# Kernel optimization log

Hardware: AMD Instinct MI355X
Metric: run time of the kernel (lower is better)

## Reference

```python
import jax, jax.numpy as jnp
import numpy as np

D_MODEL = 512
D_STATE = 128
D_CONV = 4
EXPAND = 2
HEADDIM = 64
D_INNER = EXPAND * D_MODEL            # 1024
NHEADS = D_INNER // HEADDIM           # 16
CONV_DIM = D_INNER + 2 * D_STATE      # 1280
D_IN_PROJ = 2 * D_INNER + 2 * D_STATE + NHEADS  # 2320
EPS = 1e-5


def _mamba2(u, in_w, conv_w, conv_b, A_log, dt_bias, Dp, norm_w, out_w):
    # u: [b, l, d_model]  -- Mamba2 forward (ngroups=1), SSD in exact quadratic form
    b, l, _ = u.shape
    zxbcdt = u @ in_w.T                                   # [b,l,2320]
    z = zxbcdt[..., :D_INNER]
    xBC = zxbcdt[..., D_INNER:D_INNER + CONV_DIM]
    dt = zxbcdt[..., D_INNER + CONV_DIM:]                 # [b,l,nheads]
    # causal depthwise conv1d (kernel 4) + silu
    xp = jnp.pad(xBC, ((0, 0), (D_CONV - 1, 0), (0, 0)))
    conv = sum(xp[:, k:k + l, :] * conv_w[:, k] for k in range(D_CONV))
    xBC = jax.nn.silu(conv + conv_b)
    x = xBC[..., :D_INNER].reshape(b, l, NHEADS, HEADDIM)
    Bm = xBC[..., D_INNER:D_INNER + D_STATE]              # [b,l,d_state]
    Cm = xBC[..., D_INNER + D_STATE:]                     # [b,l,d_state]
    dt = jax.nn.softplus(dt + dt_bias)                    # [b,l,nheads]
    dtA = dt * (-jnp.exp(A_log))                          # [b,l,nheads], negative
    # SSD quadratic (semiseparable) form: L[t,s] = exp(sum_{r=s+1..t} dtA_r), causal
    cs = jnp.cumsum(dtA, axis=1)                          # [b,l,nh]
    seg = cs[:, :, None, :] - cs[:, None, :, :]           # [b,t,s,nh]
    mask = jnp.tril(jnp.ones((l, l), bool))
    L = jnp.exp(jnp.where(mask[None, :, :, None], seg, -jnp.inf))
    G = jnp.einsum('btd,bsd->bts', Cm, Bm)                # C_t . B_s
    dtx = dt[..., None] * x                               # [b,l,nh,hd]
    y = jnp.einsum('btsn,bsnp->btnp', G[..., None] * L, dtx)
    y = (y + x * Dp[:, None]).reshape(b, l, D_INNER)      # D skip
    # gated RMSNorm (norm_before_gate=False): rmsnorm(y * silu(z)) * weight
    y = y * jax.nn.silu(z)
    y = y * jax.lax.rsqrt(jnp.mean(jnp.square(y), -1, keepdims=True) + EPS) * norm_w
    return y @ out_w.T


def _forward(x, h_in_w, h_conv_w, h_conv_b, h_A_log, h_dt_bias, h_D, h_norm_w, h_out_w,
             v_in_w, v_conv_w, v_conv_b, v_A_log, v_dt_bias, v_D, v_norm_w, v_out_w,
             fc_w, fc_b):
    B, H, W, C = x.shape
    hp = (h_in_w, h_conv_w, h_conv_b, h_A_log, h_dt_bias, h_D, h_norm_w, h_out_w)
    vp = (v_in_w, v_conv_w, v_conv_b, v_A_log, v_dt_bias, v_D, v_norm_w, v_out_w)
    # horizontal: scan along W for each (B*H) row
    xh = x.reshape(-1, W, C)
    h1 = _mamba2(xh, *hp)
    # NOTE: original code flips dim 0 (batch), reproduced faithfully
    h2 = jnp.flip(_mamba2(jnp.flip(xh, 0), *hp), 0)
    h = jnp.concatenate([h1, h2], -1).reshape(B, H, W, -1)
    # vertical: scan along H for each (B*W) column
    xv = jnp.transpose(x, (0, 2, 1, 3)).reshape(-1, H, C)
    v1 = _mamba2(xv, *vp)
    v2 = jnp.flip(_mamba2(jnp.flip(xv, 0), *vp), 0)
    v = jnp.transpose(jnp.concatenate([v1, v2], -1).reshape(B, W, H, -1), (0, 2, 1, 3))
    out = jnp.concatenate([v, h], -1) @ fc_w.T + fc_b     # [B,H,W,C]
    return out


def setup_inputs() -> dict:
    key = jax.random.key(0)
    ks = jax.random.split(key, 8)
    B, H, W, C = 2, 64, 64, D_MODEL
    x = jax.random.normal(ks[0], (B, H, W, C), jnp.float32)

    def mk(k):
        kk = jax.random.split(k, 5)
        return {
            'in_w': 0.02 * jax.random.normal(kk[0], (D_IN_PROJ, D_MODEL), jnp.float32),
            'conv_w': 0.1 * jax.random.normal(kk[1], (CONV_DIM, D_CONV), jnp.float32),
            'conv_b': jnp.zeros((CONV_DIM,), jnp.float32),
            'A_log': jnp.log(jax.random.uniform(kk[2], (NHEADS,), jnp.float32, 1.0, 16.0)),
            'dt_bias': jnp.log(jnp.expm1(jax.random.uniform(kk[3], (NHEADS,), jnp.float32, 1e-3, 0.1))),
            'D': jnp.ones((NHEADS,), jnp.float32),
            'norm_w': jnp.ones((D_INNER,), jnp.float32),
            'out_w': 0.02 * jax.random.normal(kk[4], (D_MODEL, D_INNER), jnp.float32),
        }

    hp, vp = mk(ks[1]), mk(ks[2])
    inp = {'x': x}
    inp.update({f'h_{n}': v for n, v in hp.items()})
    inp.update({f'v_{n}': v for n, v in vp.items()})
    inp['fc_w'] = 0.02 * jax.random.normal(ks[3], (D_MODEL, 4 * D_MODEL), jnp.float32)
    inp['fc_b'] = jnp.zeros((D_MODEL,), jnp.float32)
    return inp


def reference(x, h_in_w, h_conv_w, h_conv_b, h_A_log, h_dt_bias, h_D, h_norm_w, h_out_w,
              v_in_w, v_conv_w, v_conv_b, v_A_log, v_dt_bias, v_D, v_norm_w, v_out_w,
              fc_w, fc_b):
    return _forward(x, h_in_w, h_conv_w, h_conv_b, h_A_log, h_dt_bias, h_D, h_norm_w, h_out_w,
                    v_in_w, v_conv_w, v_conv_b, v_A_log, v_dt_bias, v_D, v_norm_w, v_out_w,
                    fc_w, fc_b)
```

## Files before the change

### kernel.cpp

```cpp
#include <hip/hip_runtime.h>

#define NROWS 8192
#define NZX   2304
#define BCS   136
#define XMS   72

#define PB0 4096
#define PB1 (PB0 + 2048)
#define PB2 (PB1 + 2304)
#define PB3 (PB2 + 256)
#define PB4 (PB3 + 512)

typedef __attribute__((ext_vector_type(8))) short bf16x8;
typedef __attribute__((ext_vector_type(4))) float f32x4;

__device__ __forceinline__ float bf2f(unsigned short u) {
    union { unsigned int i; float f; } v; v.i = ((unsigned int)u) << 16; return v.f;
}
__device__ __forceinline__ unsigned short f2bf(float f) {
    union { float f; unsigned int i; } v; v.f = f;
    return (unsigned short)((v.i + 0x8000u) >> 16);
}

__device__ __forceinline__ void async_lds16(const unsigned short* g, unsigned short* l) {
    __builtin_amdgcn_global_load_lds(
        (const __attribute__((address_space(1))) unsigned int*)g,
        (__attribute__((address_space(3))) unsigned int*)l, 16, 0, 0);
}

__global__ __launch_bounds__(256) void prep_kernel(
    const float* __restrict__ x, const float* __restrict__ fcw,
    const float* __restrict__ iw0, const float* __restrict__ iw1,
    const float* __restrict__ ow0, const float* __restrict__ ow1,
    const float* __restrict__ db0, const float* __restrict__ db1,
    const float* __restrict__ al0, const float* __restrict__ al1,
    unsigned short* __restrict__ xbf, unsigned short* __restrict__ wf,
    unsigned short* __restrict__ wbA, unsigned short* __restrict__ wbOT0,
    unsigned short* __restrict__ wbOT1, float* __restrict__ dtbb,
    float* __restrict__ csbb)
{
    __shared__ char sm[37888] __attribute__((aligned(16)));
    const int blk = blockIdx.x, tid = threadIdx.x;
    if (blk < PB0) {
        int i = blk * 256 + tid;
        float4 v = *(const float4*)(x + (size_t)i * 4);
        ushort4 o;
        o.x = f2bf(v.x); o.y = f2bf(v.y); o.z = f2bf(v.z); o.w = f2bf(v.w);
        *(ushort4*)(xbf + (size_t)i * 4) = o;
    } else if (blk < PB1) {
        int idx = (blk - PB0) * 256 + tid;
        int o = idx >> 10, c = idx & 1023;
        int half = c >> 9, cc = c & 511;
        float v = fcw[(size_t)o * 2048 + half * 1024 + cc] +
                  fcw[(size_t)o * 2048 + half * 1024 + 512 + cc];
        wf[idx] = f2bf(v);
    } else if (blk < PB2) {
        int local = blk - PB1;
        int dir = local / 1152;
        int i = (local % 1152) * 256 + tid;
        const float* s = dir ? iw1 : iw0;
        float4 v = *(const float4*)(s + (size_t)i * 4);
        ushort4 o;
        o.x = f2bf(v.x); o.y = f2bf(v.y); o.z = f2bf(v.z); o.w = f2bf(v.w);
        *(ushort4*)(wbA + (size_t)dir * (2304 * 512) + (size_t)i * 4) = o;
    } else if (blk < PB3) {
        float (*T)[65] = (float(*)[65])sm;
        int local = blk - PB2;
        int z = local >> 7, rem = local & 127;
        const float* s = z ? ow1 : ow0;
        unsigned short* d = z ? wbOT1 : wbOT0;
        const int bo = (rem >> 4) * 64, bc = (rem & 15) * 64;
#pragma unroll
        for (int i = 0; i < 16; ++i) {
            int slot = tid + i * 256;
            int r = slot >> 6, c = slot & 63;
            T[r][c] = s[(size_t)(bo + r) * 1024 + bc + c];
        }
        __syncthreads();
#pragma unroll
        for (int i = 0; i < 16; ++i) {
            int slot = tid + i * 256;
            int cr = slot >> 6, oc = slot & 63;
            d[(size_t)(bc + cr) * 512 + bo + oc] = f2bf(T[oc][cr]);
        }
    } else {
        float (*wsm)[512] = (float(*)[512])sm;
        float (*xs)[68]   = (float(*)[68])(sm + 16384);
        float (*dta)[64]  = (float(*)[64])(sm + 16384 + 17408);
        float (*dtt)[64]  = (float(*)[64])(sm + 16384 + 17408 + 2048);
        int local = blk - PB3;
        const int dir = local >> 8, bxl = local & 255;
        const float* in_w = dir ? iw1 : iw0;
        const float* dt_bias = dir ? db1 : db0;
        const float* A_log = dir ? al1 : al0;
        float* dtb = dtbb + (size_t)dir * 131072;
        float* csb = csbb + (size_t)dir * 131072;
        const int seq = bxl >> 1, hq = bxl & 1;
#pragma unroll
        for (int i = 0; i < 4; ++i) {
            int slot = tid + i * 256;
            int h = slot >> 7, c = (slot & 127) * 4;
            *(float4*)&wsm[h][c] = *(const float4*)(in_w + (size_t)(2304 + hq * 8 + h) * 512 + c);
        }
        const int t = tid & 63, hg = tid >> 6;
        float acc[2] = {0.f, 0.f};
        for (int c0 = 0; c0 < 512; c0 += 64) {
            __syncthreads();
#pragma unroll
            for (int i = 0; i < 4; ++i) {
                int slot = tid + i * 256;
                int r = slot >> 4, cc = (slot & 15) * 4;
                size_t row = (dir == 0) ? (size_t)seq * 64 + r
                                        : (size_t)(seq >> 6) * 4096 + (size_t)r * 64 + (seq & 63);
                *(float4*)&xs[r][cc] = *(const float4*)(x + row * 512 + c0 + cc);
            }
            __syncthreads();
#pragma unroll
            for (int cc = 0; cc < 64; cc += 4) {
                float4 u4 = *(const float4*)&xs[t][cc];
                const float* w0 = &wsm[hg * 2][c0 + cc];
                const float* w1 = &wsm[hg * 2 + 1][c0 + cc];
                acc[0] += u4.x * w0[0] + u4.y * w0[1] + u4.z * w0[2] + u4.w * w0[3];
                acc[1] += u4.x * w1[0] + u4.y * w1[1] + u4.z * w1[2] + u4.w * w1[3];
            }
        }
#pragma unroll
        for (int hh = 0; hh < 2; ++hh) {
            int hl = hg * 2 + hh;
            int h = hq * 8 + hl;
            float v = acc[hh] + dt_bias[h];
            float dtv = (v > 20.f) ? v : log1pf(__expf(v));
            dtt[hl][t] = dtv;
            dta[hl][t] = dtv * -__expf(A_log[h]);
        }
        __syncthreads();
        if (tid < 8) {
            float run = 0.f;
            int ob = (seq * 16 + hq * 8 + tid) * 64;
            for (int tt = 0; tt < 64; ++tt) {
                run += dta[tid][tt];
                dtb[ob + tt] = dtt[tid][tt];
                csb[ob + tt] = run;
            }
        }
    }
}

__global__ __launch_bounds__(256) void gemm_phase(
    const unsigned short* __restrict__ xbf, const unsigned short* __restrict__ wbA,
    unsigned short* __restrict__ zx, const unsigned short* __restrict__ wf,
    const unsigned short* __restrict__ wbOT0, const unsigned short* __restrict__ wbOT1,
    unsigned short* __restrict__ wcomb)
{
    __shared__ unsigned short SMEM[16384];
    unsigned short* As = SMEM;
    unsigned short* Bs = SMEM + 8192;
    const int bx = blockIdx.x, by = blockIdx.y, z = blockIdx.z;
    const unsigned short *A, *B;
    unsigned short* C;
    int lda, ldb, ldc, perm, mB, nB;
    if (bx < 64) {
        A = xbf; lda = 512; perm = z;
        B = wbA + (size_t)z * (2304 * 512); ldb = 512;
        C = zx + (size_t)z * NROWS * NZX; ldc = NZX;
        mB = bx * 128; nB = by * 128;
    } else {
        if (by >= 8) return;
        A = z ? wf : wf + 512; lda = 1024; perm = 0;
        B = z ? wbOT1 : wbOT0; ldb = 512;
        C = z ? wcomb : wcomb + 1024; ldc = 2048;
        mB = (bx - 64) * 128; nB = by * 128;
    }
    const int tid = threadIdx.x, wave = tid >> 6, lane = tid & 63;
    const int wm = (wave >> 1) * 64, wn = (wave & 1) * 64;
    const int lr = lane & 15, lq = lane >> 4;
    const unsigned short* AgP[4];
    const unsigned short* BgP[4];
    unsigned short* lA[4];
    unsigned short* lB[4];
#pragma unroll
    for (int i = 0; i < 4; ++i) {
        int s = tid + i * 256;
        int r = s >> 3, p = s & 7;
        int q = p ^ (r & 7);
        int ar = mB + r;
        if (perm) ar = (ar & ~4095) | ((ar & 63) << 6) | ((ar >> 6) & 63);
        AgP[i] = A + (size_t)ar * lda + q * 8;
        BgP[i] = B + (size_t)(nB + r) * ldb + q * 8;
        lA[i] = As + s * 8;
        lB[i] = Bs + s * 8;
    }
    const int aswz = lr & 7;
    int arb[4], brb[4];
#pragma unroll
    for (int i = 0; i < 4; ++i) {
        arb[i] = (wm + i * 16 + lr) * 64;
        brb[i] = (wn + i * 16 + lr) * 64;
    }
    f32x4 zero4 = {0.f,0.f,0.f,0.f};
    f32x4 acc[4][4] = {{zero4,zero4,zero4,zero4},{zero4,zero4,zero4,zero4},
                       {zero4,zero4,zero4,zero4},{zero4,zero4,zero4,zero4}};
    for (int k0 = 0; k0 < 512; k0 += 64) {
#pragma unroll
        for (int i = 0; i < 4; ++i) async_lds16(AgP[i] + k0, lA[i]);
#pragma unroll
        for (int i = 0; i < 4; ++i) async_lds16(BgP[i] + k0, lB[i]);
        __syncthreads();
#pragma unroll
        for (int kh = 0; kh < 2; ++kh) {
            const int ksw = ((kh * 4 + lq) ^ aswz) * 8;
            bf16x8 a[4], b[4];
#pragma unroll
            for (int i = 0; i < 4; ++i) a[i] = *(const bf16x8*)(As + arb[i] + ksw);
#pragma unroll
            for (int i = 0; i < 4; ++i) b[i] = *(const bf16x8*)(Bs + brb[i] + ksw);
#pragma unroll
            for (int mi = 0; mi < 4; ++mi)
#pragma unroll
                for (int ni = 0; ni < 4; ++ni)
                    acc[mi][ni] = __builtin_amdgcn_mfma_f32_16x16x32_bf16(
                        a[mi], b[ni], acc[mi][ni], 0, 0, 0);
        }
        __syncthreads();
    }
    unsigned short* WR = SMEM + wave * 1024;
#pragma unroll
    for (int mi = 0; mi < 4; ++mi) {
#pragma unroll
        for (int ni = 0; ni < 4; ++ni) {
#pragma unroll
            for (int r = 0; r < 4; ++r) {
                int r16 = lq * 4 + r;
                int cn = ni * 16 + lr;
                int gp = ((cn >> 3) + (r16 >> 1)) & 7;
                WR[r16 * 64 + gp * 8 + (cn & 7)] = f2bf(acc[mi][ni][r]);
            }
        }
#pragma unroll
        for (int j = 0; j < 2; ++j) {
            int r16 = j * 8 + (lane >> 3);
            int gr = lane & 7;
            int gp = (gr + (r16 >> 1)) & 7;
            uint4 v = *(const uint4*)(WR + r16 * 64 + gp * 8);
            int row = mB + wm + mi * 16 + r16;
            *(uint4*)(C + (size_t)row * ldc + nB + wn + gr * 8) = v;
        }
    }
}

__global__ __launch_bounds__(256) void gemm_final2048(
    const unsigned short* __restrict__ YV, const unsigned short* __restrict__ YH,
    const unsigned short* __restrict__ W, const float* __restrict__ bias,
    float* __restrict__ C)
{
    __shared__ unsigned short As[128 * 64];
    __shared__ unsigned short Bs[64 * 64];
    const int tid = threadIdx.x, wave = tid >> 6, lane = tid & 63;
    const int mB = blockIdx.x * 128, nB = blockIdx.y * 64;
    const int lr = lane & 15, lq = lane >> 4;
    int aq[4], agr[4], apr[4];
    unsigned short* lA[4];
    const unsigned short* BgP[2];
    unsigned short* lB[2];
#pragma unroll
    for (int i = 0; i < 4; ++i) {
        int s = tid + i * 256;
        int r = s >> 3, p = s & 7;
        aq[i] = (p ^ (r & 7)) * 8;
        int gr = mB + r;
        agr[i] = gr;
        apr[i] = (gr & ~4095) | ((gr & 63) << 6) | ((gr >> 6) & 63);
        lA[i] = As + s * 8;
    }
#pragma unroll
    for (int i = 0; i < 2; ++i) {
        int s = tid + i * 256;
        int r = s >> 3, p = s & 7;
        int q = p ^ (r & 7);
        BgP[i] = W + (size_t)(nB + r) * 2048 + q * 8;
        lB[i] = Bs + s * 8;
    }
    const int aswz = lr & 7;
    int arb[2], brb[4];
#pragma unroll
    for (int i = 0; i < 2; ++i) arb[i] = (wave * 32 + i * 16 + lr) * 64;
#pragma unroll
    for (int i = 0; i < 4; ++i) brb[i] = (i * 16 + lr) * 64;
    f32x4 zero4 = {0.f,0.f,0.f,0.f};
    f32x4 acc[2][4] = {{zero4,zero4,zero4,zero4},{zero4,zero4,zero4,zero4}};
    for (int k0 = 0; k0 < 2048; k0 += 64) {
#pragma unroll
        for (int i = 0; i < 4; ++i) {
            int kk = k0 + aq[i];
            const unsigned short* g = (kk < 1024)
                ? YV + (size_t)apr[i] * 1024 + kk
                : YH + (size_t)agr[i] * 1024 + (kk - 1024);
            async_lds16(g, lA[i]);
        }
#pragma unroll
        for (int i = 0; i < 2; ++i) async_lds16(BgP[i] + k0, lB[i]);
        __syncthreads();
#pragma unroll
        for (int kh = 0; kh < 2; ++kh) {
            const int ksw = ((kh * 4 + lq) ^ aswz) * 8;
            bf16x8 a[2], b[4];
#pragma unroll
            for (int i = 0; i < 2; ++i) a[i] = *(const bf16x8*)(As + arb[i] + ksw);
#pragma unroll
            for (int i = 0; i < 4; ++i) b[i] = *(const bf16x8*)(Bs + brb[i] + ksw);
#pragma unroll
            for (int mi = 0; mi < 2; ++mi)
#pragma unroll
                for (int ni = 0; ni < 4; ++ni)
                    acc[mi][ni] = __builtin_amdgcn_mfma_f32_16x16x32_bf16(
                        a[mi], b[ni], acc[mi][ni], 0, 0, 0);
        }
        __syncthreads();
    }
    const int rbase = lq * 4;
#pragma unroll
    for (int mi = 0; mi < 2; ++mi)
#pragma unroll
        for (int ni = 0; ni < 4; ++ni) {
            int col = nB + ni * 16 + lr;
            float bb = bias[col];
#pragma unroll
            for (int r = 0; r < 4; ++r) {
                int row = mB + wave * 32 + mi * 16 + rbase + r;
                C[(size_t)row * 512 + col] = acc[mi][ni][r] + bb;
            }
        }
}

__global__ __launch_bounds__(320) void conv_silu(
    const unsigned short* __restrict__ zxb, const float* __restrict__ cw0,
    const float* __restrict__ cw1, const float* __restrict__ cb0,
    const float* __restrict__ cb1, unsigned short* __restrict__ xbcb)
{
    __shared__ unsigned short S[64 * 320];
    const int dir = blockIdx.y;
    const unsigned short* zx = zxb + (size_t)dir * NROWS * NZX;
    unsigned short* xbc = xbcb + (size_t)dir * NROWS * 1280;
    const float* cw = dir ? cw1 : cw0;
    const float* cb = dir ? cb1 : cb0;
    const int tid = threadIdx.x;
    const int seq = blockIdx.x >> 2, tile = blockIdx.x & 3;
    const int cbase = tile * 320;
    const unsigned short* src = zx + (size_t)seq * 64 * NZX + 1024 + cbase;
#pragma unroll
    for (int i = 0; i < 8; ++i) {
        int slot = tid + i * 320;
        int r = slot / 40, ch = (slot % 40) * 8;
        *(uint4*)(S + r * 320 + ch) = *(const uint4*)(src + (size_t)r * NZX + ch);
    }
    __syncthreads();
    const int c8 = (tid % 40) * 8, rg = tid / 40;
    const int gc = cbase + c8;
    float4 b0 = *(const float4*)(cb + gc), b1 = *(const float4*)(cb + gc + 4);
    const float bias[8] = {b0.x,b0.y,b0.z,b0.w,b1.x,b1.y,b1.z,b1.w};
    float4 wv[8];
#pragma unroll
    for (int j = 0; j < 8; ++j) wv[j] = *(const float4*)(cw + (size_t)(gc + j) * 4);
    unsigned short* dst = xbc + (size_t)seq * 64 * 1280 + gc;
#pragma unroll
    for (int r = 0; r < 8; ++r) {
        int t = rg * 8 + r;
        float acc[8];
#pragma unroll
        for (int j = 0; j < 8; ++j) acc[j] = bias[j];
#pragma unroll
        for (int k = 0; k < 4; ++k) {
            int ts = t + k - 3;
            if (ts >= 0) {
                uint4 xv = *(const uint4*)(S + ts * 320 + c8);
                const unsigned short* xs = (const unsigned short*)&xv;
#pragma unroll
                for (int j = 0; j < 8; ++j)
                    acc[j] += bf2f(xs[j]) * ((const float*)&wv[j])[k];
            }
        }
        unsigned short out8[8] __attribute__((aligned(16)));
#pragma unroll
        for (int j = 0; j < 8; ++j) out8[j] = f2bf(acc[j] / (1.f + __expf(-acc[j])));
        *(uint4*)(dst + (size_t)t * 1280) = *(const uint4*)out8;
    }
}

__global__ __launch_bounds__(256) void gmat_kernel(
    const unsigned short* __restrict__ xbcb, float* __restrict__ Gbuf)
{
    __shared__ unsigned short Bs[64 * BCS];
    __shared__ unsigned short Cs[64 * BCS];
    const int dir = blockIdx.y, seq = blockIdx.x;
    const unsigned short* base = xbcb + (size_t)dir * NROWS * 1280
                                      + (size_t)seq * 64 * 1280;
    const int tid = threadIdx.x;
    const int lane = tid & 63, wave = tid >> 6;
#pragma unroll
    for (int i = 0; i < 4; ++i) {
        int e = (tid + i * 256) * 8;
        int r = e >> 7, c = e & 127;
        *(uint4*)(Bs + r * BCS + c) = *(const uint4*)(base + (size_t)r * 1280 + 1024 + c);
        *(uint4*)(Cs + r * BCS + c) = *(const uint4*)(base + (size_t)r * 1280 + 1152 + c);
    }
    __syncthreads();
    const int lr = lane & 15, lq = lane >> 4;
    f32x4 zero4 = {0.f,0.f,0.f,0.f};
    f32x4 acc[4] = {zero4, zero4, zero4, zero4};
#pragma unroll
    for (int kt = 0; kt < 4; ++kt) {
        bf16x8 a = *(const bf16x8*)(Cs + (wave * 16 + lr) * BCS + kt * 32 + lq * 8);
#pragma unroll
        for (int ni = 0; ni < 4; ++ni) {
            bf16x8 b = *(const bf16x8*)(Bs + (ni * 16 + lr) * BCS + kt * 32 + lq * 8);
            acc[ni] = __builtin_amdgcn_mfma_f32_16x16x32_bf16(a, b, acc[ni], 0, 0, 0);
        }
    }
    float* G = Gbuf + ((size_t)dir * 128 + seq) * 4096;
#pragma unroll
    for (int ni = 0; ni < 4; ++ni) {
        int s = ni * 16 + lr;
#pragma unroll
        for (int r = 0; r < 4; ++r) {
            int t = wave * 16 + lq * 4 + r;
            G[t * 64 + s] = acc[ni][r];
        }
    }
}

__global__ __launch_bounds__(256) void scan_kernel(
    const unsigned short* __restrict__ xbcb, const float* __restrict__ Gbuf,
    const float* __restrict__ dtbb, const float* __restrict__ csbb,
    const float* __restrict__ Dv0, const float* __restrict__ Dv1,
    unsigned short* __restrict__ yh, unsigned short* __restrict__ yv)
{
    __shared__ unsigned short XsT[64 * XMS];
    __shared__ unsigned short Ms[64 * XMS];
    __shared__ float dts[64], css[64];
    const int dir = blockIdx.y;
    const unsigned short* xbc = xbcb + (size_t)dir * NROWS * 1280;
    const float* dtb = dtbb + (size_t)dir * 131072;
    const float* csb = csbb + (size_t)dir * 131072;
    const float* Dv = dir ? Dv1 : Dv0;
    unsigned short* y = dir ? yv : yh;
    const int tid = threadIdx.x;
    const int lane = tid & 63, wave = tid >> 6;
    const int seq = blockIdx.x >> 4, h = blockIdx.x & 15;
    if (tid < 64) {
        dts[tid] = dtb[(seq * 16 + h) * 64 + tid];
        css[tid] = csb[(seq * 16 + h) * 64 + tid];
    }
    const unsigned short* base = xbc + (size_t)seq * 64 * 1280;
#pragma unroll
    for (int i = 0; i < 2; ++i) {
        int e = (tid + i * 256) * 8;
        int t = e >> 6, p0 = e & 63;
        uint4 xval = *(const uint4*)(base + (size_t)t * 1280 + h * 64 + p0);
        const unsigned short* xs = (const unsigned short*)&xval;
#pragma unroll
        for (int j = 0; j < 8; ++j) {
            int jl = (j + lane) & 7;
            XsT[(p0 + jl) * XMS + t] = xs[jl];
        }
    }
    const int lr = lane & 15, lq = lane >> 4;
    const float* G = Gbuf + ((size_t)dir * 128 + seq) * 4096;
    f32x4 acc[4];
#pragma unroll
    for (int ni = 0; ni < 4; ++ni) {
        int s = ni * 16 + lr;
#pragma unroll
        for (int r = 0; r < 4; ++r) {
            int t = wave * 16 + lq * 4 + r;
            acc[ni][r] = G[t * 64 + s];
        }
    }
    __syncthreads();
    float css_t[4];
#pragma unroll
    for (int r = 0; r < 4; ++r) css_t[r] = css[wave * 16 + lq * 4 + r];
#pragma unroll
    for (int ni = 0; ni < 4; ++ni) {
        int s = ni * 16 + lr;
        float cs_s = css[s], dt_s = dts[s];
#pragma unroll
        for (int r = 0; r < 4; ++r) {
            int t = wave * 16 + lq * 4 + r;
            float e = __expf(fminf(css_t[r] - cs_s, 0.f));
            float m = (s <= t) ? acc[ni][r] * e * dt_s : 0.f;
            Ms[t * XMS + s] = f2bf(m);
        }
    }
    __syncthreads();
    f32x4 zero4 = {0.f,0.f,0.f,0.f};
    f32x4 yacc[4] = {zero4, zero4, zero4, zero4};
#pragma unroll
    for (int kt = 0; kt < 2; ++kt) {
        bf16x8 a = *(const bf16x8*)(Ms + (wave * 16 + lr) * XMS + kt * 32 + lq * 8);
#pragma unroll
        for (int ni = 0; ni < 4; ++ni) {
            bf16x8 b = *(const bf16x8*)(XsT + (ni * 16 + lr) * XMS + kt * 32 + lq * 8);
            yacc[ni] = __builtin_amdgcn_mfma_f32_16x16x32_bf16(a, b, yacc[ni], 0, 0, 0);
        }
    }
    const float Dh = Dv[h];
#pragma unroll
    for (int ni = 0; ni < 4; ++ni) {
        int p = ni * 16 + lr;
#pragma unroll
        for (int r = 0; r < 4; ++r) {
            int t = wave * 16 + lq * 4 + r;
            float v = yacc[ni][r] + Dh * bf2f(XsT[p * XMS + t]);
            Ms[t * XMS + p] = f2bf(v);
        }
    }
    __syncthreads();
    unsigned short* yout = y + (size_t)seq * 64 * 1024 + h * 64;
#pragma unroll
    for (int i = 0; i < 2; ++i) {
        int slot = tid + i * 256;
        int t = slot >> 3, pc = (slot & 7) * 8;
        uint4 v = *(const uint4*)(Ms + t * XMS + pc);
        *(uint4*)(yout + (size_t)t * 1024 + pc) = v;
    }
}

__global__ __launch_bounds__(128) void gate_norm(
    const unsigned short* __restrict__ zxb, unsigned short* __restrict__ yh,
    unsigned short* __restrict__ yv, const float* __restrict__ nw0,
    const float* __restrict__ nw1)
{
    const int dir = blockIdx.y;
    const unsigned short* zx = zxb + (size_t)dir * NROWS * NZX;
    unsigned short* y = dir ? yv : yh;
    const float* nw = dir ? nw1 : nw0;
    const int row = blockIdx.x, tid = threadIdx.x;
    uint4 yv4 = *(const uint4*)(y + (size_t)row * 1024 + tid * 8);
    uint4 zv4 = *(const uint4*)(zx + (size_t)row * NZX + tid * 8);
    const unsigned short* ys = (const unsigned short*)&yv4;
    const unsigned short* zs = (const unsigned short*)&zv4;
    float g[8]; float ss = 0.f;
#pragma unroll
    for (int j = 0; j < 8; ++j) {
        float zv = bf2f(zs[j]);
        float gv = bf2f(ys[j]) * (zv / (1.f + __expf(-zv)));
        g[j] = gv; ss += gv * gv;
    }
#pragma unroll
    for (int off = 32; off > 0; off >>= 1) ss += __shfl_xor(ss, off, 64);
    __shared__ float red[2];
    if ((tid & 63) == 0) red[tid >> 6] = ss;
    __syncthreads();
    ss = red[0] + red[1];
    const float scale = rsqrtf(ss * (1.f / 1024.f) + 1e-5f);
    unsigned short out8[8] __attribute__((aligned(16)));
#pragma unroll
    for (int j = 0; j < 8; ++j) out8[j] = f2bf(g[j] * scale * nw[tid * 8 + j]);
    *(uint4*)(y + (size_t)row * 1024 + tid * 8) = *(const uint4*)out8;
}

extern "C" void kernel_launch(void* const* d_in, const int* in_sizes, int n_in,
                              void* d_out, int out_size, void* d_ws, size_t ws_size,
                              hipStream_t stream)
{
    (void)in_sizes; (void)n_in; (void)out_size; (void)ws_size;
    const float* x   = (const float*)d_in[0];
    const float* fcw = (const float*)d_in[17];
    const float* fcb = (const float*)d_in[18];
    const float* iw0 = (const float*)d_in[1];  const float* iw1 = (const float*)d_in[9];
    const float* cw0 = (const float*)d_in[2];  const float* cw1 = (const float*)d_in[10];
    const float* cb0 = (const float*)d_in[3];  const float* cb1 = (const float*)d_in[11];
    const float* al0 = (const float*)d_in[4];  const float* al1 = (const float*)d_in[12];
    const float* db0 = (const float*)d_in[5];  const float* db1 = (const float*)d_in[13];
    const float* Dv0 = (const float*)d_in[6];  const float* Dv1 = (const float*)d_in[14];
    const float* nw0 = (const float*)d_in[7];  const float* nw1 = (const float*)d_in[15];
    const float* ow0 = (const float*)d_in[8];  const float* ow1 = (const float*)d_in[16];

    char* ws = (char*)d_ws;
    size_t off = 0;
    auto alloc = [&](size_t bytes) {
        void* p = ws + off; off += (bytes + 255) & ~(size_t)255; return p;
    };
    unsigned short* xbf   = (unsigned short*)alloc((size_t)NROWS * 512 * 2);
    unsigned short* wbA   = (unsigned short*)alloc((size_t)2 * 2304 * 512 * 2);
    unsigned short* wbOT0 = (unsigned short*)alloc((size_t)1024 * 512 * 2);
    unsigned short* wbOT1 = (unsigned short*)alloc((size_t)1024 * 512 * 2);
    unsigned short* wf    = (unsigned short*)alloc((size_t)512 * 1024 * 2);
    unsigned short* wcomb = (unsigned short*)alloc((size_t)512 * 2048 * 2);
    unsigned short* zx    = (unsigned short*)alloc((size_t)2 * NROWS * NZX * 2);
    unsigned short* xbc   = (unsigned short*)alloc((size_t)2 * NROWS * 1280 * 2);
    float* Gbuf           = (float*)alloc((size_t)2 * 128 * 4096 * 4);
    float* dtb            = (float*)alloc((size_t)2 * 2048 * 64 * 4);
    float* csb            = (float*)alloc((size_t)2 * 2048 * 64 * 4);
    unsigned short* ybh   = (unsigned short*)alloc((size_t)NROWS * 1024 * 2);
    unsigned short* ybv   = (unsigned short*)alloc((size_t)NROWS * 1024 * 2);

    prep_kernel<<<PB4, 256, 0, stream>>>(x, fcw, iw0, iw1, ow0, ow1, db0, db1,
                                         al0, al1, xbf, wf, wbA, wbOT0, wbOT1,
                                         dtb, csb);
    gemm_phase<<<dim3(68, 18, 2), 256, 0, stream>>>(xbf, wbA, zx, wf,
                                                    wbOT0, wbOT1, wcomb);
    conv_silu<<<dim3(512, 2), 320, 0, stream>>>(zx, cw0, cw1, cb0, cb1, xbc);
    gmat_kernel<<<dim3(128, 2), 256, 0, stream>>>(xbc, Gbuf);
    scan_kernel<<<dim3(2048, 2), 256, 0, stream>>>(xbc, Gbuf, dtb, csb,
                                                   Dv0, Dv1, ybh, ybv);
    gate_norm<<<dim3(NROWS, 2), 128, 0, stream>>>(zx, ybh, ybv, nw0, nw1);
    gemm_final2048<<<dim3(64, 8), 256, 0, stream>>>(ybv, ybh, wcomb, fcb, (float*)d_out);
}
```

Baseline: 290.2 us.

## Fuse causal conv+SiLU into in-proj GEMM epilogue and remap blocks for XCD locality

Removes the separate conv_silu kernel. The in-projection GEMM epilogue now applies the depthwise causal conv and SiLU directly to output tiles in the xBC column range, writing xbc without a round trip through zx. This works because each 64-row sequence is fully contained in a wave's 64-row tile. Block-index remapping is also added to group M tiles per XCD in both GEMMs, and the weight-combine blocks move to an extra grid row. The cost is a heavier epilogue with more registers and LDS traffic in those blocks.

```diff
diff --git a/kernel.cpp b/kernel.cpp
--- a/kernel.cpp
+++ b/kernel.cpp
@@ -150,26 +150,32 @@
     const unsigned short* __restrict__ xbf, const unsigned short* __restrict__ wbA,
     unsigned short* __restrict__ zx, const unsigned short* __restrict__ wf,
     const unsigned short* __restrict__ wbOT0, const unsigned short* __restrict__ wbOT1,
-    unsigned short* __restrict__ wcomb)
+    unsigned short* __restrict__ wcomb, const float* __restrict__ cw0,
+    const float* __restrict__ cw1, const float* __restrict__ cb0,
+    const float* __restrict__ cb1, unsigned short* __restrict__ xbc)
 {
     __shared__ unsigned short SMEM[16384];
     unsigned short* As = SMEM;
     unsigned short* Bs = SMEM + 8192;
     const int bx = blockIdx.x, by = blockIdx.y, z = blockIdx.z;
+    const int inproj = (by < 18);
     const unsigned short *A, *B;
     unsigned short* C;
     int lda, ldb, ldc, perm, mB, nB;
-    if (bx < 64) {
+    if (inproj) {
+        int did = by * 64 + bx;
+        int xcd = did & 7, l = did >> 3;
+        mB = (xcd * 8 + (l & 7)) * 128;
+        nB = (l >> 3) * 128;
         A = xbf; lda = 512; perm = z;
         B = wbA + (size_t)z * (2304 * 512); ldb = 512;
         C = zx + (size_t)z * NROWS * NZX; ldc = NZX;
-        mB = bx * 128; nB = by * 128;
     } else {
-        if (by >= 8) return;
+        if (bx >= 32) return;
         A = z ? wf : wf + 512; lda = 1024; perm = 0;
         B = z ? wbOT1 : wbOT0; ldb = 512;
         C = z ? wcomb : wcomb + 1024; ldc = 2048;
-        mB = (bx - 64) * 128; nB = by * 128;
+        mB = (bx >> 3) * 128; nB = (bx & 7) * 128;
     }
     const int tid = threadIdx.x, wave = tid >> 6, lane = tid & 63;
     const int wm = (wave >> 1) * 64, wn = (wave & 1) * 64;
@@ -223,27 +229,90 @@
         }
         __syncthreads();
     }
-    unsigned short* WR = SMEM + wave * 1024;
-#pragma unroll
-    for (int mi = 0; mi < 4; ++mi) {
-#pragma unroll
-        for (int ni = 0; ni < 4; ++ni) {
-#pragma unroll
-            for (int r = 0; r < 4; ++r) {
-                int r16 = lq * 4 + r;
-                int cn = ni * 16 + lr;
-                int gp = ((cn >> 3) + (r16 >> 1)) & 7;
-                WR[r16 * 64 + gp * 8 + (cn & 7)] = f2bf(acc[mi][ni][r]);
-            }
-        }
-#pragma unroll
-        for (int j = 0; j < 2; ++j) {
-            int r16 = j * 8 + (lane >> 3);
-            int gr = lane & 7;
-            int gp = (gr + (r16 >> 1)) & 7;
-            uint4 v = *(const uint4*)(WR + r16 * 64 + gp * 8);
-            int row = mB + wm + mi * 16 + r16;
-            *(uint4*)(C + (size_t)row * ldc + nB + wn + gr * 8) = v;
+    if (inproj && nB >= 1024) {
+        unsigned short* WT = SMEM + wave * 4096;
+#pragma unroll
+        for (int mi = 0; mi < 4; ++mi)
+#pragma unroll
+            for (int ni = 0; ni < 4; ++ni)
+#pragma unroll
+                for (int r = 0; r < 4; ++r)
+                    WT[(mi * 16 + lq * 4 + r) * 64 + ni * 16 + lr] =
+                        f2bf(acc[mi][ni][r]);
+        const int rg = lane >> 3, cg = lane & 7;
+        const int ch = (nB - 1024) + wn + cg * 8;
+        const float* cwp = z ? cw1 : cw0;
+        const float* cbp = z ? cb1 : cb0;
+        float w0[8], w1[8], w2[8], w3[8], bb[8];
+#pragma unroll
+        for (int j = 0; j < 8; ++j) {
+            float4 wv = *(const float4*)(cwp + (size_t)(ch + j) * 4);
+            w0[j] = wv.x; w1[j] = wv.y; w2[j] = wv.z; w3[j] = wv.w;
+        }
+        {
+            float4 b0 = *(const float4*)(cbp + ch);
+            float4 b1 = *(const float4*)(cbp + ch + 4);
+            bb[0]=b0.x; bb[1]=b0.y; bb[2]=b0.z; bb[3]=b0.w;
+            bb[4]=b1.x; bb[5]=b1.y; bb[6]=b1.z; bb[7]=b1.w;
+        }
+        float p1[8], p2[8], p3[8];
+        if (rg == 0) {
+#pragma unroll
+            for (int j = 0; j < 8; ++j) { p1[j] = 0.f; p2[j] = 0.f; p3[j] = 0.f; }
+        } else {
+            bf16x8 v1 = *(const bf16x8*)(WT + (rg * 8 - 1) * 64 + cg * 8);
+            bf16x8 v2 = *(const bf16x8*)(WT + (rg * 8 - 2) * 64 + cg * 8);
+            bf16x8 v3 = *(const bf16x8*)(WT + (rg * 8 - 3) * 64 + cg * 8);
+#pragma unroll
+            for (int j = 0; j < 8; ++j) {
+                p1[j] = bf2f((unsigned short)v1[j]);
+                p2[j] = bf2f((unsigned short)v2[j]);
+                p3[j] = bf2f((unsigned short)v3[j]);
+            }
+        }
+        unsigned short* xo = xbc + (size_t)z * NROWS * 1280
+                           + (size_t)(mB + wm) * 1280 + ch;
+#pragma unroll
+        for (int rr = 0; rr < 8; ++rr) {
+            int row = rg * 8 + rr;
+            bf16x8 cv = *(const bf16x8*)(WT + row * 64 + cg * 8);
+            float cur[8];
+#pragma unroll
+            for (int j = 0; j < 8; ++j) cur[j] = bf2f((unsigned short)cv[j]);
+            unsigned short o8[8] __attribute__((aligned(16)));
+#pragma unroll
+            for (int j = 0; j < 8; ++j) {
+                float a = bb[j] + w3[j] * cur[j] + w2[j] * p1[j]
+                        + w1[j] * p2[j] + w0[j] * p3[j];
+                o8[j] = f2bf(a / (1.f + __expf(-a)));
+            }
+            *(uint4*)(xo + (size_t)row * 1280) = *(const uint4*)o8;
+#pragma unroll
+            for (int j = 0; j < 8; ++j) { p3[j] = p2[j]; p2[j] = p1[j]; p1[j] = cur[j]; }
+        }
+    } else {
+        unsigned short* WR = SMEM + wave * 1024;
+#pragma unroll
+        for (int mi = 0; mi < 4; ++mi) {
+#pragma unroll
+            for (int ni = 0; ni < 4; ++ni) {
+#pragma unroll
+                for (int r = 0; r < 4; ++r) {
+                    int r16 = lq * 4 + r;
+                    int cn = ni * 16 + lr;
+                    int gp = ((cn >> 3) + (r16 >> 1)) & 7;
+                    WR[r16 * 64 + gp * 8 + (cn & 7)] = f2bf(acc[mi][ni][r]);
+                }
+            }
+#pragma unroll
+            for (int j = 0; j < 2; ++j) {
+                int r16 = j * 8 + (lane >> 3);
+                int gr = lane & 7;
+                int gp = (gr + (r16 >> 1)) & 7;
+                uint4 v = *(const uint4*)(WR + r16 * 64 + gp * 8);
+                int row = mB + wm + mi * 16 + r16;
+                *(uint4*)(C + (size_t)row * ldc + nB + wn + gr * 8) = v;
+            }
         }
     }
 }
@@ -256,7 +325,8 @@
     __shared__ unsigned short As[128 * 64];
     __shared__ unsigned short Bs[64 * 64];
     const int tid = threadIdx.x, wave = tid >> 6, lane = tid & 63;
-    const int mB = blockIdx.x * 128, nB = blockIdx.y * 64;
+    const int did = blockIdx.y * 64 + blockIdx.x;
+    const int mB = (did >> 3) * 128, nB = (did & 7) * 64;
     const int lr = lane & 15, lq = lane >> 4;
     int aq[4], agr[4], apr[4];
     unsigned short* lA[4];
@@ -330,60 +400,6 @@
                 C[(size_t)row * 512 + col] = acc[mi][ni][r] + bb;
             }
         }
-}
-
-__global__ __launch_bounds__(320) void conv_silu(
-    const unsigned short* __restrict__ zxb, const float* __restrict__ cw0,
-    const float* __restrict__ cw1, const float* __restrict__ cb0,
-    const float* __restrict__ cb1, unsigned short* __restrict__ xbcb)
-{
-    __shared__ unsigned short S[64 * 320];
-    const int dir = blockIdx.y;
-    const unsigned short* zx = zxb + (size_t)dir * NROWS * NZX;
-    unsigned short* xbc = xbcb + (size_t)dir * NROWS * 1280;
-    const float* cw = dir ? cw1 : cw0;
-    const float* cb = dir ? cb1 : cb0;
-    const int tid = threadIdx.x;
-    const int seq = blockIdx.x >> 2, tile = blockIdx.x & 3;
-    const int cbase = tile * 320;
-    const unsigned short* src = zx + (size_t)seq * 64 * NZX + 1024 + cbase;
-#pragma unroll
-    for (int i = 0; i < 8; ++i) {
-        int slot = tid + i * 320;
-        int r = slot / 40, ch = (slot % 40) * 8;
-        *(uint4*)(S + r * 320 + ch) = *(const uint4*)(src + (size_t)r * NZX + ch);
-    }
-    __syncthreads();
-    const int c8 = (tid % 40) * 8, rg = tid / 40;
-    const int gc = cbase + c8;
-    float4 b0 = *(const float4*)(cb + gc), b1 = *(const float4*)(cb + gc + 4);
-    const float bias[8] = {b0.x,b0.y,b0.z,b0.w,b1.x,b1.y,b1.z,b1.w};
-    float4 wv[8];
-#pragma unroll
-    for (int j = 0; j < 8; ++j) wv[j] = *(const float4*)(cw + (size_t)(gc + j) * 4);
-    unsigned short* dst = xbc + (size_t)seq * 64 * 1280 + gc;
-#pragma unroll
-    for (int r = 0; r < 8; ++r) {
-        int t = rg * 8 + r;
-        float acc[8];
-#pragma unroll
-        for (int j = 0; j < 8; ++j) acc[j] = bias[j];
-#pragma unroll
-        for (int k = 0; k < 4; ++k) {
-            int ts = t + k - 3;
-            if (ts >= 0) {
-                uint4 xv = *(const uint4*)(S + ts * 320 + c8);
-                const unsigned short* xs = (const unsigned short*)&xv;
-#pragma unroll
-                for (int j = 0; j < 8; ++j)
-                    acc[j] += bf2f(xs[j]) * ((const float*)&wv[j])[k];
-            }
-        }
-        unsigned short out8[8] __attribute__((aligned(16)));
-#pragma unroll
-        for (int j = 0; j < 8; ++j) out8[j] = f2bf(acc[j] / (1.f + __expf(-acc[j])));
-        *(uint4*)(dst + (size_t)t * 1280) = *(const uint4*)out8;
-    }
 }
 
 __global__ __launch_bounds__(256) void gmat_kernel(
@@ -598,9 +614,9 @@
     prep_kernel<<<PB4, 256, 0, stream>>>(x, fcw, iw0, iw1, ow0, ow1, db0, db1,
                                          al0, al1, xbf, wf, wbA, wbOT0, wbOT1,
                                          dtb, csb);
-    gemm_phase<<<dim3(68, 18, 2), 256, 0, stream>>>(xbf, wbA, zx, wf,
-                                                    wbOT0, wbOT1, wcomb);
-    conv_silu<<<dim3(512, 2), 320, 0, stream>>>(zx, cw0, cw1, cb0, cb1, xbc);
+    gemm_phase<<<dim3(64, 19, 2), 256, 0, stream>>>(xbf, wbA, zx, wf,
+                                                    wbOT0, wbOT1, wcomb,
+                                                    cw0, cw1, cb0, cb1, xbc);
     gmat_kernel<<<dim3(128, 2), 256, 0, stream>>>(xbc, Gbuf);
     scan_kernel<<<dim3(2048, 2), 256, 0, stream>>>(xbc, Gbuf, dtb, csb,
                                                    Dv0, Dv1, ybh, ybv);
```

Result: faster. 282.2 us (-2.8%).
